# Kernel tuning notes

Measured on AMD Instinct MI355X. Metric: run time of the kernel, lower is better.

The kernel has to match this reference:

```python
import jax, jax.numpy as jnp
import numpy as np

B, C, H, W = 8, 512, 64, 64
HID = 4 * C  # MixFFN hidden = in_dim*4
FOCUS = 3.0


def _ln(x, g, b, eps=1e-5):
    m = x.mean(-1, keepdims=True)
    v = ((x - m) ** 2).mean(-1, keepdims=True)
    return (x - m) / jnp.sqrt(v + eps) * g + b


def setup_inputs() -> dict:
    key = jax.random.key(0)
    ks = jax.random.split(key, 12)
    init = lambda k, shape, fan: (jax.random.normal(k, shape, jnp.float32) / np.float32(np.sqrt(fan)))
    d = {}
    d['x'] = jax.random.normal(ks[0], (B, C, H, W), jnp.float32)
    # 1x1 conv weights stored as (Cout, Cin)
    d['Wq'] = init(ks[1], (C, C), C); d['bq'] = jnp.zeros((C,), jnp.float32)
    d['Wk'] = init(ks[2], (C, C), C); d['bk'] = jnp.zeros((C,), jnp.float32)
    d['Wv'] = init(ks[3], (C, C), C); d['bv'] = jnp.zeros((C,), jnp.float32)
    d['scale'] = jnp.zeros((1, 1, C), jnp.float32)  # nn.Parameter(torch.zeros)
    # MixFFN_skip params
    d['fc1_w'] = init(ks[4], (C, HID), C); d['fc1_b'] = jnp.zeros((HID,), jnp.float32)
    d['dw_w'] = init(ks[5], (HID, 1, 3, 3), 9); d['dw_b'] = jnp.zeros((HID,), jnp.float32)
    d['fc2_w'] = init(ks[6], (HID, C), HID); d['fc2_b'] = jnp.zeros((C,), jnp.float32)
    d['ln1_g'] = jnp.ones((HID,), jnp.float32); d['ln1_b'] = jnp.zeros((HID,), jnp.float32)
    d['lnm_g'] = jnp.ones((C,), jnp.float32); d['lnm_b'] = jnp.zeros((C,), jnp.float32)
    return d


def _forward(x, Wq, bq, Wk, bk, Wv, bv, scale, fc1_w, fc1_b, dw_w, dw_b, fc2_w, fc2_b, ln1_g, ln1_b, lnm_g, lnm_b):
    b, c, h, w = x.shape
    n = h * w
    # 1x1 convs (NCHW), then RAW reshape to (B, N, C) as in torch (no permute!)
    conv1 = lambda t, Wm, bm: jnp.einsum('bchw,oc->bohw', t, Wm) + bm[None, :, None, None]
    q = jax.nn.softmax(conv1(x, Wq, bq).reshape(b, n, c), axis=1)
    k = jax.nn.softmax(conv1(x, Wk, bk).reshape(b, n, c), axis=2)
    v = conv1(x, Wv, bv).reshape(b, n, c)
    q = jax.nn.relu(q) + 1e-6
    k = jax.nn.relu(k) + 1e-6
    sc = jax.nn.softplus(scale)
    q = q / sc
    k = k / sc
    q_norm = jnp.linalg.norm(q, axis=-1, keepdims=True)
    k_norm = jnp.linalg.norm(k, axis=-1, keepdims=True)
    q = q ** FOCUS  # focusing_factor <= 6 branch
    k = k ** FOCUS
    q = q / jnp.linalg.norm(q, axis=-1, keepdims=True) * q_norm
    k = k / jnp.linalg.norm(k, axis=-1, keepdims=True) * k_norm
    # num_heads == 1: (b h) n c == b n c
    z = 1.0 / (jnp.einsum('bic,bc->bi', q, k.sum(axis=1)) + 1e-6)
    kv = jnp.einsum('bjc,bjd->bcd', k, v)  # O(N) linear attention summary
    attn = jnp.einsum('bic,bcd,bi->bid', q, kv, z)
    shortcut = jnp.transpose(x, (0, 2, 3, 1)).reshape(b, n, c)  # proper rearrange b c h w -> b (h w) c
    enhanced = shortcut + attn
    # MixFFN_skip(norm_mlp(enhanced), h, w)
    t = _ln(enhanced, lnm_g, lnm_b)
    a = t @ fc1_w + fc1_b  # (B, N, HID)
    ai = jnp.transpose(a, (0, 2, 1)).reshape(b, HID, h, w)
    dw = jax.lax.conv_general_dilated(ai, dw_w, (1, 1), 'SAME',
                                      dimension_numbers=('NCHW', 'OIHW', 'NCHW'),
                                      feature_group_count=HID)
    dw = dw + dw_b[None, :, None, None]
    dw = jnp.transpose(dw.reshape(b, HID, n), (0, 2, 1))
    ax = jax.nn.gelu(_ln(dw + a, ln1_g, ln1_b), approximate=False)
    mlp_out = ax @ fc2_w + fc2_b
    out = enhanced + mlp_out
    return out.reshape(b, h, w, c)


def reference(x, Wq, bq, Wk, bk, Wv, bv, scale, fc1_w, fc1_b, dw_w, dw_b, fc2_w, fc2_b, ln1_g, ln1_b, lnm_g, lnm_b):
    return _forward(x, Wq, bq, Wk, bk, Wv, bv, scale, fc1_w, fc1_b, dw_w, dw_b, fc2_w, fc2_b, ln1_g, ln1_b, lnm_g, lnm_b)
```

## Files before the change

### kernel.cpp

```cpp
#include <hip/hip_runtime.h>
#include <hip/hip_bf16.h>

typedef __hip_bfloat16 bf16;
typedef __attribute__((ext_vector_type(8))) short bh8;
typedef __attribute__((ext_vector_type(4))) float f32x4;

#define CDIM 512
#define NDIM 4096
#define HIDD 2048
#define BATCH 8

__device__ __forceinline__ float bf2f(short s) {
    union { unsigned u; float f; } c; c.u = ((unsigned)(unsigned short)s) << 16; return c.f;
}
__device__ __forceinline__ short f2bf(float f) {
    union { __hip_bfloat16 h; short s; } c; c.h = __float2bfloat16(f); return c.s;
}
__device__ __forceinline__ float wsum(float v) {
#pragma unroll
    for (int o = 32; o; o >>= 1) v += __shfl_xor(v, o);
    return v;
}
__device__ __forceinline__ float wmax(float v) {
#pragma unroll
    for (int o = 32; o; o >>= 1) v = fmaxf(v, __shfl_xor(v, o));
    return v;
}

#define GLL(g, l) __builtin_amdgcn_global_load_lds( \
    (const __attribute__((address_space(1))) unsigned int*)(g), \
    (__attribute__((address_space(3))) unsigned int*)(l), 16, 0, 0)


__device__ __forceinline__ void stage_ht(const bf16* __restrict__ base, int ld,
                                         int kt, char* ldsb, int t) {
#pragma unroll
    for (int l = 0; l < 2; ++l) {
        const int id = l * 512 + t;
        const int row = id >> 3, c = id & 7;
        const int cs = c ^ (row & 7);
        GLL(base + (long)row * ld + kt + (cs << 3),
            ldsb + l * 8192 + (t >> 6) * 1024 + (t & 63) * 16);
    }
}

template<int MODE, int MFAST>
__global__ __launch_bounds__(512, 2)
void gemm256(const bf16* __restrict__ A, int lda, long sA,
             const bf16* __restrict__ Bt, int ldb, long sB,
             void* __restrict__ Cp, int ldc, long sC, int K,
             const float* __restrict__ bias,
             void* __restrict__ aux1, void* __restrict__ aux2)
{
    __shared__ __align__(16) bf16 smem[65536];
    char* smemB = (char*)smem;
    int bx, by, bz;
    {
        const int gx = gridDim.x, gy = gridDim.y;
        const int nwg = gx * gy * gridDim.z;
        int lid = blockIdx.x + gx * (blockIdx.y + gy * blockIdx.z);
        const int cpx = nwg >> 3;
        int swz = (lid & 7) * cpx + (lid >> 3);
        if constexpr (MFAST) {
            by = swz % gy; swz /= gy;
            bx = swz % gx;
            bz = swz / gx;
        } else {
            bx = swz % gx; swz /= gx;
            by = swz % gy;
            bz = swz / gy;
        }
    }
    const bf16* Ab = A + (long)bz * sA + (long)by * 256 * lda;
    const bf16* Bb = Bt + (long)bz * sB + (long)bx * 256 * ldb;
    const int t = threadIdx.x, lane = t & 63, wid = t >> 6;
    const int wm = wid >> 2, wn = wid & 3;
    const int lg = lane >> 4, lr = lane & 15;

    f32x4 acc[8][4];
#pragma unroll
    for (int m = 0; m < 8; ++m)
#pragma unroll
        for (int n = 0; n < 4; ++n) acc[m][n] = (f32x4){0.f, 0.f, 0.f, 0.f};

    const int T = K >> 6;
    stage_ht(Bb, ldb, 0, smemB + 65536, t);
    stage_ht(Bb + (long)128 * ldb, ldb, 0, smemB + 65536 + 16384, t);
    stage_ht(Ab, lda, 0, smemB, t);
    stage_ht(Ab + (long)128 * lda, lda, 0, smemB + 16384, t);

    for (int tt = 0; tt < T; ++tt) {
        const int cur = tt & 1, nb = cur ^ 1;
        const int ktn = (tt + 1) << 6;
        const bool pf = (tt + 1 < T);
        const int aco = cur ? 16384 : 0;
        const int bco = 32768 + (cur ? 16384 : 0);
        const int anb = nb ? 32768 : 0;
        const int bnb = 65536 + (nb ? 32768 : 0);

        bh8 afA[4], afB[4], bfA[4], bfB[4];

        if (pf) stage_ht(Bb, ldb, ktn, smemB + bnb, t);
        if (pf) asm volatile("s_waitcnt vmcnt(2)" ::: "memory");
        else    asm volatile("s_waitcnt vmcnt(0)" ::: "memory");
        __builtin_amdgcn_s_barrier();
#pragma unroll
        for (int m = 0; m < 4; ++m) {
            const int row = wm * 128 + m * 16 + lr;
            afA[m] = *(const bh8*)(smem + aco + row * 64 + (lg ^ (row & 7)) * 8);
        }
#pragma unroll
        for (int n = 0; n < 4; ++n) {
            const int row = wn * 64 + n * 16 + lr;
            bfA[n] = *(const bh8*)(smem + bco + row * 64 + (lg ^ (row & 7)) * 8);
        }
        asm volatile("s_waitcnt lgkmcnt(0)" ::: "memory");
        __builtin_amdgcn_sched_barrier(0);
        __builtin_amdgcn_s_setprio(1);
#pragma unroll
        for (int m = 0; m < 4; ++m)
#pragma unroll
            for (int n = 0; n < 4; ++n)
                acc[m][n] = __builtin_amdgcn_mfma_f32_16x16x32_bf16(afA[m], bfA[n], acc[m][n], 0, 0, 0);
        __builtin_amdgcn_s_setprio(0);
        __builtin_amdgcn_s_barrier();

#pragma unroll
        for (int m = 0; m < 4; ++m) {
            const int row = wm * 128 + 64 + m * 16 + lr;
            afB[m] = *(const bh8*)(smem + aco + row * 64 + (lg ^ (row & 7)) * 8);
        }
        if (pf) stage_ht(Bb + (long)128 * ldb, ldb, ktn, smemB + bnb + 16384, t);
        asm volatile("s_waitcnt lgkmcnt(0)" ::: "memory");
        __builtin_amdgcn_sched_barrier(0);
        __builtin_amdgcn_s_setprio(1);
#pragma unroll
        for (int m = 0; m < 4; ++m)
#pragma unroll
            for (int n = 0; n < 4; ++n)
                acc[4 + m][n] = __builtin_amdgcn_mfma_f32_16x16x32_bf16(afB[m], bfA[n], acc[4 + m][n], 0, 0, 0);
        __builtin_amdgcn_s_setprio(0);
        __builtin_amdgcn_s_barrier();

#pragma unroll
        for (int m = 0; m < 4; ++m) {
            const int row = wm * 128 + m * 16 + lr;
            afA[m] = *(const bh8*)(smem + aco + row * 64 + ((4 + lg) ^ (row & 7)) * 8);
        }
#pragma unroll
        for (int n = 0; n < 4; ++n) {
            const int row = wn * 64 + n * 16 + lr;
            bfB[n] = *(const bh8*)(smem + bco + row * 64 + ((4 + lg) ^ (row & 7)) * 8);
        }
        if (pf) stage_ht(Ab, lda, ktn, smemB + anb, t);
        asm volatile("s_waitcnt lgkmcnt(0)" ::: "memory");
        __builtin_amdgcn_sched_barrier(0);
        __builtin_amdgcn_s_setprio(1);
#pragma unroll
        for (int m = 0; m < 4; ++m)
#pragma unroll
            for (int n = 0; n < 4; ++n)
                acc[m][n] = __builtin_amdgcn_mfma_f32_16x16x32_bf16(afA[m], bfB[n], acc[m][n], 0, 0, 0);
        __builtin_amdgcn_s_setprio(0);
        __builtin_amdgcn_s_barrier();

#pragma unroll
        for (int m = 0; m < 4; ++m) {
            const int row = wm * 128 + 64 + m * 16 + lr;
            afB[m] = *(const bh8*)(smem + aco + row * 64 + ((4 + lg) ^ (row & 7)) * 8);
        }
        if (pf) stage_ht(Ab + (long)128 * lda, lda, ktn, smemB + anb + 16384, t);
        asm volatile("s_waitcnt lgkmcnt(0)" ::: "memory");
        __builtin_amdgcn_sched_barrier(0);
        __builtin_amdgcn_s_setprio(1);
#pragma unroll
        for (int m = 0; m < 4; ++m)
#pragma unroll
            for (int n = 0; n < 4; ++n)
                acc[4 + m][n] = __builtin_amdgcn_mfma_f32_16x16x32_bf16(afB[m], bfB[n], acc[4 + m][n], 0, 0, 0);
        __builtin_amdgcn_s_setprio(0);
        __builtin_amdgcn_s_barrier();
    }

    const int gr0 = by * 256 + wm * 128;
    const int gc0 = bx * 256 + wn * 64;
    if constexpr (MODE == 0) {
        const int which = by >> 1;
        bf16* dst = (which == 0) ? (bf16*)Cp : (which == 1) ? (bf16*)aux1 : (bf16*)aux2;
        dst += (long)bz * sC;
#pragma unroll
        for (int m = 0; m < 8; ++m)
#pragma unroll
            for (int n = 0; n < 4; ++n) {
                const int col = gc0 + n * 16 + lr;
#pragma unroll
                for (int r = 0; r < 4; ++r) {
                    const int grow = gr0 + m * 16 + lg * 4 + r;
                    float v = acc[m][n][r] + bias[grow];
                    if (which == 0) v = __expf(v);
                    dst[(long)(grow - which * 512) * ldc + col] = __float2bfloat16(v);
                }
            }
    } else {
        bf16* dst = (bf16*)Cp + (long)bz * sC;
#pragma unroll
        for (int m = 0; m < 8; ++m)
#pragma unroll
            for (int n = 0; n < 4; ++n) {
                const int col = gc0 + n * 16 + lr;
                const float bc = bias[col];
#pragma unroll
                for (int r = 0; r < 4; ++r) {
                    const int grow = gr0 + m * 16 + lg * 4 + r;
                    dst[(long)grow * ldc + col] = __float2bfloat16(acc[m][n][r] + bc);
                }
            }
    }
}

enum { EP_BF16_BROW = 1, EP_ATTN = 3, EP_BF16_BCOL = 4, EP_OUT = 5 };

template<int MODE, int TM, int MFAST>
__global__ __launch_bounds__(256)
void gemm_bt(const bf16* __restrict__ A, int lda, long sA,
             const bf16* __restrict__ Bt, int ldb, long sB,
             void* __restrict__ Cp, int ldc, long sC, int K,
             const float* __restrict__ bias,
             const void* __restrict__ aux1, long sAux1,
             const void* __restrict__ aux2, long sAux2)
{
    constexpr int MF = TM / 32;
    __shared__ __align__(16) bf16 smem[TM * 64 + 128 * 64];
    bf16* As = smem;
    bf16* Bs = smem + TM * 64;
    int bx, by, bz;
    {
        const int gx = gridDim.x, gy = gridDim.y;
        const int nwg = gx * gy * gridDim.z;
        int lid = blockIdx.x + gx * (blockIdx.y + gy * blockIdx.z);
        const int cpx = nwg >> 3;
        int swz = (lid & 7) * cpx + (lid >> 3);
        if constexpr (MFAST) {
            by = swz % gy; swz /= gy;
            bx = swz % gx;
            bz = swz / gx;
        } else {
            bx = swz % gx; swz /= gx;
            by = swz % gy;
            bz = swz / gy;
        }
    }
    const bf16* Ab = A + (long)bz * sA + (long)by * TM * lda;
    const bf16* Bb = Bt + (long)bz * sB + (long)bx * 128 * ldb;
    const int t = threadIdx.x, lane = t & 63, wid = t >> 6;
    const int wm = wid >> 1, wn = wid & 1, lg = lane >> 4, lr = lane & 15;

    f32x4 acc[MF][4];
#pragma unroll
    for (int m = 0; m < MF; ++m)
#pragma unroll
        for (int n = 0; n < 4; ++n) acc[m][n] = (f32x4){0.f, 0.f, 0.f, 0.f};

    for (int kt = 0; kt < K; kt += 64) {
#pragma unroll
        for (int i = 0; i < MF; ++i) {
            const int ch = i * 256 + t;
            const int row = ch >> 3;
            const int cs = (ch & 7) ^ (row & 7);
            GLL(Ab + (long)row * lda + kt + (cs << 3), (char*)As + i * 4096 + wid * 1024);
        }
#pragma unroll
        for (int i = 0; i < 4; ++i) {
            const int ch = i * 256 + t;
            const int row = ch >> 3;
            const int cs = (ch & 7) ^ (row & 7);
            GLL(Bb + (long)row * ldb + kt + (cs << 3), (char*)Bs + i * 4096 + wid * 1024);
        }
        __syncthreads();
#pragma unroll
        for (int kk = 0; kk < 2; ++kk) {
            bh8 af[MF], bfv[4];
#pragma unroll
            for (int m = 0; m < MF; ++m) {
                const int row = wm * (TM / 2) + m * 16 + lr;
                const int kc = (kk * 4 + lg) ^ (row & 7);
                af[m] = *(const bh8*)(As + row * 64 + kc * 8);
            }
#pragma unroll
            for (int n = 0; n < 4; ++n) {
                const int row = wn * 64 + n * 16 + lr;
                const int kc = (kk * 4 + lg) ^ (row & 7);
                bfv[n] = *(const bh8*)(Bs + row * 64 + kc * 8);
            }
#pragma unroll
            for (int m = 0; m < MF; ++m)
#pragma unroll
                for (int n = 0; n < 4; ++n)
                    acc[m][n] = __builtin_amdgcn_mfma_f32_16x16x32_bf16(af[m], bfv[n], acc[m][n], 0, 0, 0);
        }
        __syncthreads();
    }

    const int gr0 = by * TM + wm * (TM / 2);
    const int gc0 = bx * 128 + wn * 64;
#pragma unroll
    for (int m = 0; m < MF; ++m) {
#pragma unroll
        for (int n = 0; n < 4; ++n) {
            const int gc = gc0 + n * 16 + lr;
#pragma unroll
            for (int r = 0; r < 4; ++r) {
                const int gr = gr0 + m * 16 + lg * 4 + r;
                float v = acc[m][n][r];
                if constexpr (MODE == EP_BF16_BROW) {
                    ((bf16*)Cp + (long)bz * sC)[(long)gr * ldc + gc] = __float2bfloat16(v + bias[gr]);
                } else if constexpr (MODE == EP_ATTN) {
                    const bf16* xg = (const bf16*)aux1 + (long)bz * sAux1;
                    const float* zg = (const float*)aux2 + (long)bz * sAux2;
                    ((float*)Cp + (long)bz * sC)[(long)gr * ldc + gc] =
                        zg[gr] * v + bf2f(*(const short*)(xg + (long)gr * 512 + gc));
                } else if constexpr (MODE == EP_BF16_BCOL) {
                    ((bf16*)Cp + (long)bz * sC)[(long)gr * ldc + gc] = __float2bfloat16(v + bias[gc]);
                } else {
                    float* op = (float*)Cp;
                    const long idx = (long)gr * ldc + gc;
                    op[idx] = v + bias[gc] + ((const float*)aux1)[idx];
                }
            }
        }
    }
}

__global__ __launch_bounds__(256)
void gemm_tn_splitk(const bf16* __restrict__ A, int lda, long sA,
                    const bf16* __restrict__ B, int ldb, long sB,
                    bf16* __restrict__ part)
{
    __shared__ __align__(16) short smem[2 * 64 * 128];
    short* As = smem;
    short* Bs = smem + 64 * 128;
    int bx, by, bzl;
    {
        const int gx = gridDim.x, gy = gridDim.y;
        const int nwg = gx * gy * gridDim.z;
        int lid = blockIdx.x + gx * (blockIdx.y + gy * blockIdx.z);
        const int cpx = nwg >> 3;
        int swz = (lid & 7) * cpx + (lid >> 3);
        bx = swz % gx; swz /= gx;
        by = swz % gy;
        bzl = swz / gy;
    }
    const int bz = bzl >> 2, ks = bzl & 3;
    const bf16* Ab = A + (long)bz * sA + (long)ks * 1024 * lda + by * 128;
    const bf16* Bb = B + (long)bz * sB + (long)ks * 1024 * ldb + bx * 128;
    const int t = threadIdx.x, lane = t & 63, wid = t >> 6;
    const int wm = wid >> 1, wn = wid & 1, lg = lane >> 4, lr = lane & 15;

    f32x4 acc[4][4];
#pragma unroll
    for (int m = 0; m < 4; ++m)
#pragma unroll
        for (int n = 0; n < 4; ++n) acc[m][n] = (f32x4){0.f, 0.f, 0.f, 0.f};

    for (int kt = 0; kt < 1024; kt += 64) {
#pragma unroll
        for (int i = 0; i < 4; ++i) {
            const int ch = i * 256 + t;
            const int row = ch >> 4;
            const int cs = (ch & 15) ^ (((row >> 3) & 3) << 1);
            GLL(Ab + (long)(kt + row) * lda + (cs << 3), (char*)As + i * 4096 + wid * 1024);
            GLL(Bb + (long)(kt + row) * ldb + (cs << 3), (char*)Bs + i * 4096 + wid * 1024);
        }
        __syncthreads();
#pragma unroll
        for (int kk = 0; kk < 2; ++kk) {
            bh8 af[4], bfv[4];
#pragma unroll
            for (int m = 0; m < 4; ++m) {
                const int col = wm * 64 + m * 16 + lr;
#pragma unroll
                for (int u = 0; u < 8; ++u) {
                    const int row = kk * 32 + lg * 8 + u;
                    af[m][u] = As[row * 128 + (((col >> 3) ^ (((row >> 3) & 3) << 1)) << 3) + (col & 7)];
                }
            }
#pragma unroll
            for (int n = 0; n < 4; ++n) {
                const int col = wn * 64 + n * 16 + lr;
#pragma unroll
                for (int u = 0; u < 8; ++u) {
                    const int row = kk * 32 + lg * 8 + u;
                    bfv[n][u] = Bs[row * 128 + (((col >> 3) ^ (((row >> 3) & 3) << 1)) << 3) + (col & 7)];
                }
            }
#pragma unroll
            for (int m = 0; m < 4; ++m)
#pragma unroll
                for (int n = 0; n < 4; ++n)
                    acc[m][n] = __builtin_amdgcn_mfma_f32_16x16x32_bf16(af[m], bfv[n], acc[m][n], 0, 0, 0);
        }
        __syncthreads();
    }

    bf16* Cs = (bf16*)smem;
    bf16* dstb = part + ((long)bzl << 18) + (long)by * 128 * 512;
#pragma unroll
    for (int m = 0; m < 4; ++m)
#pragma unroll
        for (int n = 0; n < 4; ++n)
#pragma unroll
            for (int r = 0; r < 4; ++r) {
                const int row = wm * 64 + m * 16 + lg * 4 + r;
                const int col = wn * 64 + n * 16 + lr;
                Cs[row * 128 + (col ^ (((row >> 2) & 3) << 4))] = __float2bfloat16(acc[m][n][r]);
            }
    __syncthreads();
#pragma unroll
    for (int it = 0; it < 8; ++it) {
        const int id = it * 256 + t;
        const int row = id >> 4, colc = (id & 15) << 3;
        bh8 v = *(const bh8*)(Cs + row * 128 + (colc ^ (((row >> 2) & 3) << 4)));
        *(bh8*)(dstb + (long)row * 512 + bx * 128 + colc) = v;
    }
}

__global__ __launch_bounds__(256)
void k_transpose3(const float* __restrict__ fc1w, bf16* __restrict__ fc1wT,
                  const float* __restrict__ fc2w, bf16* __restrict__ fc2wT,
                  const float* __restrict__ x, bf16* __restrict__ xbT)
{
    __shared__ float tile[64][65];
    const int bid = blockIdx.x;
    const float* s; bf16* d; int Rd, Cd, bx, by;
    if (bid < 256) {
        s = fc1w; d = fc1wT; Rd = 2048; Cd = 512; bx = bid & 31; by = bid >> 5;
    } else if (bid < 512) {
        const int i = bid - 256;
        s = fc2w; d = fc2wT; Rd = 512; Cd = 2048; bx = i & 7; by = i >> 3;
    } else {
        const int i = bid - 512;
        const int bz = i >> 9, j = i & 511;
        bx = j & 63; by = j >> 6;
        const long NC = (long)NDIM * CDIM;
        s = x + (long)bz * NC; d = xbT + (long)bz * NC; Rd = 4096; Cd = 512;
    }
    const int r0 = bx * 64, c0 = by * 64;
    const int t = threadIdx.x;
#pragma unroll 4
    for (int i = 0; i < 16; ++i) {
        int idx = i * 256 + t;
        int a = idx >> 6, b = idx & 63;
        tile[a][b] = s[(long)(c0 + a) * Rd + r0 + b];
    }
    __syncthreads();
#pragma unroll 4
    for (int i = 0; i < 16; ++i) {
        int idx = i * 256 + t;
        int a = idx >> 6, b = idx & 63;
        d[(long)(r0 + a) * Cd + c0 + b] = __float2bfloat16(tile[b][a]);
    }
}

__global__ void k_setup(const float* __restrict__ Wq, const float* __restrict__ Wk,
                        const float* __restrict__ Wv, bf16* __restrict__ oq,
                        bf16* __restrict__ ok, bf16* __restrict__ ov,
                        const float* __restrict__ scale, float* __restrict__ invsc,
                        const float* __restrict__ w, float* __restrict__ wT,
                        const float* __restrict__ bq, const float* __restrict__ bk,
                        const float* __restrict__ bv, float* __restrict__ bqkv) {
    int i = blockIdx.x * 256 + threadIdx.x;
    if (i < 262144) {
        oq[i] = __float2bfloat16(Wq[i]);
        ok[i] = __float2bfloat16(Wk[i]);
        ov[i] = __float2bfloat16(Wv[i]);
    }
    if (i < 512) invsc[i] = 1.0f / log1pf(expf(scale[i]));
    if (i < 1536) bqkv[i] = (i < 512 ? bq[i] : (i < 1024 ? bk[i - 512] : bv[i - 1024]));
    if (i < HIDD * 9) {
        int chn = i / 9, kk = i % 9;
        wT[kk * HIDD + chn] = w[i];
    }
}

__global__ void k_fill(float* o, int n, float v) {
    int i = blockIdx.x * 256 + threadIdx.x; if (i < n) o[i] = v;
}

__global__ __launch_bounds__(256)
void k_colsums(const bf16* __restrict__ qe, const bf16* __restrict__ kb,
               float* __restrict__ qpart, float* __restrict__ kpart) {
    const int xb = blockIdx.x;
    const int ic = blockIdx.y, b = blockIdx.z;
    const int j = (xb & 1) * 256 + threadIdx.x;
    const bf16* src = (xb < 2) ? qe : kb;
    const bf16* p = src + (long)b * (NDIM * CDIM) + (long)ic * 256 * CDIM + j;
    float s = 0.f;
    for (int i = 0; i < 256; ++i) s += bf2f(*(const short*)(p + (long)i * CDIM));
    ((xb < 2) ? qpart : kpart)[((long)b * 16 + ic) * CDIM + j] = s;
}

__global__ __launch_bounds__(256)
void k_red2(const float* __restrict__ qpart, float* __restrict__ qsum,
            const float* __restrict__ kpart, float* __restrict__ ksum) {
    const int idx = blockIdx.x * 256 + threadIdx.x;
    const int which = idx >> 12, r = idx & 4095;
    const int b = r >> 9, c = r & 511;
    const float* src = which ? kpart : qpart;
    float s = 0.f;
#pragma unroll
    for (int jc = 0; jc < 16; ++jc) s += src[((long)(b * 16 + jc)) * CDIM + c];
    (which ? ksum : qsum)[r] = s;
}

__global__ __launch_bounds__(256)
void k_kvqrow(const bf16* __restrict__ part, bf16* __restrict__ kvt,
              const bf16* __restrict__ qe, const float* __restrict__ qsum,
              const float* __restrict__ invsc, bf16* __restrict__ qb,
              const float* __restrict__ ksum, float* __restrict__ z)
{
    if (blockIdx.x < 1024) {
        const long e = ((long)blockIdx.x * 256 + threadIdx.x) * 8;
        const int b = (int)(e >> 18);
        const int off = (int)(e & 262143);
        float s[8] = {0.f, 0.f, 0.f, 0.f, 0.f, 0.f, 0.f, 0.f};
#pragma unroll
        for (int ks = 0; ks < 4; ++ks) {
            bh8 v = *(const bh8*)(part + (((long)(b * 4 + ks)) << 18) + off);
#pragma unroll
            for (int j = 0; j < 8; ++j) s[j] += bf2f(v[j]);
        }
        bh8 o;
#pragma unroll
        for (int j = 0; j < 8; ++j) o[j] = f2bf(s[j]);
        *(bh8*)(kvt + ((long)b << 18) + off) = o;
        return;
    }
    const long row = (long)(blockIdx.x - 1024) * 4 + (threadIdx.x >> 6);
    const int lane = threadIdx.x & 63;
    const int b = (int)(row >> 12);
    bh8 ev = *(const bh8*)(qe + row * CDIM + lane * 8);
    const float* qs = qsum + b * CDIM + lane * 8;
    const float* is = invsc + lane * 8;
    f32x4 s0 = *(const f32x4*)qs, s1 = *(const f32x4*)(qs + 4);
    f32x4 i0 = *(const f32x4*)is, i1 = *(const f32x4*)(is + 4);
    float q[8];
#pragma unroll
    for (int k = 0; k < 4; ++k) {
        q[k]     = (bf2f(ev[k]) / s0[k] + 1e-6f) * i0[k];
        q[k + 4] = (bf2f(ev[k + 4]) / s1[k] + 1e-6f) * i1[k];
    }
    float s2 = 0.f, s6 = 0.f, q3[8];
#pragma unroll
    for (int k = 0; k < 8; ++k) { s2 += q[k] * q[k]; float c = q[k] * q[k] * q[k]; q3[k] = c; s6 += c * c; }
    s2 = wsum(s2); s6 = wsum(s6);
    const float sc = sqrtf(s2) / sqrtf(s6);
    bh8 o;
#pragma unroll
    for (int k = 0; k < 8; ++k) o[k] = f2bf(q3[k] * sc);
    *(bh8*)(qb + row * CDIM + lane * 8) = o;
    const float* ks = ksum + (long)b * CDIM + lane * 8;
    f32x4 k0 = *(const f32x4*)ks, k1 = *(const f32x4*)(ks + 4);
    float zd = 0.f;
#pragma unroll
    for (int j = 0; j < 4; ++j) { zd += bf2f(o[j]) * k0[j]; zd += bf2f(o[j + 4]) * k1[j]; }
    zd = wsum(zd);
    if (lane == 0) z[row] = 1.0f / (zd + 1e-6f);
}

__global__ __launch_bounds__(256)
void k_krow(bf16* __restrict__ kb, const float* __restrict__ invsc)
{
    const long row = (long)blockIdx.x * 4 + (threadIdx.x >> 6);
    const int lane = threadIdx.x & 63;
    bh8 v = *(const bh8*)(kb + row * CDIM + lane * 8);
    const float* is = invsc + lane * 8;
    f32x4 i0 = *(const f32x4*)is, i1 = *(const f32x4*)(is + 4);
    float xv[8];
#pragma unroll
    for (int k = 0; k < 8; ++k) xv[k] = bf2f(v[k]);
    float mx = -1e30f;
#pragma unroll
    for (int k = 0; k < 8; ++k) mx = fmaxf(mx, xv[k]);
    mx = wmax(mx);
    float e[8], se = 0.f;
#pragma unroll
    for (int k = 0; k < 8; ++k) { e[k] = __expf(xv[k] - mx); se += e[k]; }
    se = wsum(se);
    const float inv = 1.0f / se;
    float q[8];
#pragma unroll
    for (int k = 0; k < 4; ++k) {
        q[k]     = (e[k] * inv + 1e-6f) * i0[k];
        q[k + 4] = (e[k + 4] * inv + 1e-6f) * i1[k];
    }
    float s2 = 0.f, s6 = 0.f, q3[8];
#pragma unroll
    for (int k = 0; k < 8; ++k) { s2 += q[k] * q[k]; float c = q[k] * q[k] * q[k]; q3[k] = c; s6 += c * c; }
    s2 = wsum(s2); s6 = wsum(s6);
    const float sc = sqrtf(s2) / sqrtf(s6);
    bh8 o;
#pragma unroll
    for (int k = 0; k < 8; ++k) o[k] = f2bf(q3[k] * sc);
    *(bh8*)(kb + row * CDIM + lane * 8) = o;
}

__global__ __launch_bounds__(256)
void k_ln512(const float* __restrict__ src, const float* __restrict__ g,
             const float* __restrict__ bta, bf16* __restrict__ dst)
{
    const long row = (long)blockIdx.x * 4 + (threadIdx.x >> 6);
    const int lane = threadIdx.x & 63;
    const float* p = src + row * CDIM + lane * 8;
    f32x4 a0 = *(const f32x4*)p, a1 = *(const f32x4*)(p + 4);
    float s = 0.f, ss = 0.f;
#pragma unroll
    for (int k = 0; k < 4; ++k) { s += a0[k] + a1[k]; ss += a0[k] * a0[k] + a1[k] * a1[k]; }
    s = wsum(s); ss = wsum(ss);
    const float mean = s * (1.0f / 512), var = ss * (1.0f / 512) - mean * mean;
    const float rstd = rsqrtf(var + 1e-5f);
    const float* gp = g + lane * 8;
    const float* bp = bta + lane * 8;
    f32x4 g0 = *(const f32x4*)gp, g1 = *(const f32x4*)(gp + 4);
    f32x4 b0 = *(const f32x4*)bp, b1 = *(const f32x4*)(bp + 4);
    bh8 o;
#pragma unroll
    for (int k = 0; k < 4; ++k) {
        o[k]     = f2bf((a0[k] - mean) * rstd * g0[k] + b0[k]);
        o[k + 4] = f2bf((a1[k] - mean) * rstd * g1[k] + b1[k]);
    }
    *(bh8*)(dst + row * CDIM + lane * 8) = o;
}

__global__ __launch_bounds__(256)
void k_dwlngelu4(const bf16* __restrict__ a, const float* __restrict__ dwwT,
                 const float* __restrict__ dwb, const float* __restrict__ g1,
                 const float* __restrict__ b1, bf16* __restrict__ ax)
{
    const long s0 = (long)blockIdx.x * 4;
    const int h = (int)((s0 >> 6) & 63);
    const int w0 = (int)(s0 & 63);
    const int ch = threadIdx.x * 8;

    float wgt[9][8];
#pragma unroll
    for (int kk = 0; kk < 9; ++kk) {
        f32x4 w0v = *(const f32x4*)(dwwT + kk * HIDD + ch);
        f32x4 w1v = *(const f32x4*)(dwwT + kk * HIDD + ch + 4);
#pragma unroll
        for (int j = 0; j < 4; ++j) { wgt[kk][j] = w0v[j]; wgt[kk][j + 4] = w1v[j]; }
    }
#pragma unroll
    for (int j = 0; j < 8; ++j) wgt[4][j] += 1.0f;

    float acc[4][8];
    {
        f32x4 d0 = *(const f32x4*)(dwb + ch), d1 = *(const f32x4*)(dwb + ch + 4);
#pragma unroll
        for (int ti = 0; ti < 4; ++ti)
#pragma unroll
            for (int j = 0; j < 4; ++j) { acc[ti][j] = d0[j]; acc[ti][j + 4] = d1[j]; }
    }

#pragma unroll
    for (int dy = -1; dy <= 1; ++dy) {
        const int hh = h + dy;
        if ((unsigned)hh >= 64u) continue;
#pragma unroll
        for (int c = -1; c <= 4; ++c) {
            const int ww = w0 + c;
            if ((unsigned)ww >= 64u) continue;
            bh8 v = *(const bh8*)(a + (s0 + (long)dy * 64 + c) * HIDD + ch);
            float f[8];
#pragma unroll
            for (int j = 0; j < 8; ++j) f[j] = bf2f(v[j]);
#pragma unroll
            for (int ti = 0; ti < 4; ++ti) {
                const int dx = c - ti;
                if (dx < -1 || dx > 1) continue;
                const int kk = (dy + 1) * 3 + (dx + 1);
#pragma unroll
                for (int j = 0; j < 8; ++j) acc[ti][j] += wgt[kk][j] * f[j];
            }
        }
    }

    float sv[4], qv[4];
#pragma unroll
    for (int ti = 0; ti < 4; ++ti) {
        float s = 0.f, q = 0.f;
#pragma unroll
        for (int j = 0; j < 8; ++j) { s += acc[ti][j]; q += acc[ti][j] * acc[ti][j]; }
        sv[ti] = wsum(s); qv[ti] = wsum(q);
    }
    __shared__ float red[4][4][2];
    const int wid = threadIdx.x >> 6, lane = threadIdx.x & 63;
    if (lane == 0)
#pragma unroll
        for (int ti = 0; ti < 4; ++ti) { red[wid][ti][0] = sv[ti]; red[wid][ti][1] = qv[ti]; }
    __syncthreads();

    f32x4 ga = *(const f32x4*)(g1 + ch), gb = *(const f32x4*)(g1 + ch + 4);
    f32x4 ba = *(const f32x4*)(b1 + ch), bb = *(const f32x4*)(b1 + ch + 4);
    float gg[8], bb8[8];
#pragma unroll
    for (int j = 0; j < 4; ++j) { gg[j] = ga[j]; gg[j + 4] = gb[j]; bb8[j] = ba[j]; bb8[j + 4] = bb[j]; }

#pragma unroll
    for (int ti = 0; ti < 4; ++ti) {
        const float s = red[0][ti][0] + red[1][ti][0] + red[2][ti][0] + red[3][ti][0];
        const float q = red[0][ti][1] + red[1][ti][1] + red[2][ti][1] + red[3][ti][1];
        const float mean = s * (1.0f / 2048), var = q * (1.0f / 2048) - mean * mean;
        const float rstd = rsqrtf(var + 1e-5f);
        bh8 o;
#pragma unroll
        for (int j = 0; j < 8; ++j) {
            float y = (acc[ti][j] - mean) * rstd * gg[j] + bb8[j];
            o[j] = f2bf(0.5f * y * (1.0f + erff(y * 0.70710678118654752f)));
        }
        *(bh8*)(ax + (s0 + ti) * HIDD + ch) = o;
    }
}

extern "C" void kernel_launch(void* const* d_in, const int* in_sizes, int n_in,
                              void* d_out, int out_size, void* d_ws, size_t ws_size,
                              hipStream_t stream) {
    const float* x     = (const float*)d_in[0];
    const float* Wq    = (const float*)d_in[1];
    const float* bq    = (const float*)d_in[2];
    const float* Wk    = (const float*)d_in[3];
    const float* bk    = (const float*)d_in[4];
    const float* Wv    = (const float*)d_in[5];
    const float* bv    = (const float*)d_in[6];
    const float* scale = (const float*)d_in[7];
    const float* fc1_w = (const float*)d_in[8];
    const float* fc1_b = (const float*)d_in[9];
    const float* dw_w  = (const float*)d_in[10];
    const float* dw_b  = (const float*)d_in[11];
    const float* fc2_w = (const float*)d_in[12];
    const float* fc2_b = (const float*)d_in[13];
    const float* ln1_g = (const float*)d_in[14];
    const float* ln1_b = (const float*)d_in[15];
    const float* lnm_g = (const float*)d_in[16];
    const float* lnm_b = (const float*)d_in[17];
    float* out = (float*)d_out;
    char* p = (char*)d_ws;

    bf16*  xbT   = (bf16*)(p + 0);
    bf16*  kb    = (bf16*)(p + 33554432);
    bf16*  vb    = (bf16*)(p + 67108864);
    bf16*  kvt   = (bf16*)(p + 100663296);
    bf16*  wqb   = (bf16*)(p + 104857600);
    bf16*  wkb   = (bf16*)(p + 105381888);
    bf16*  wvb   = (bf16*)(p + 105906176);
    bf16*  fc1wT = (bf16*)(p + 106430464);
    bf16*  fc2wT = (bf16*)(p + 108527616);
    float* invsc = (float*)(p + 110624768);
    float* dwwT  = (float*)(p + 110626816);
    float* bqkv  = (float*)(p + 110700544);
    float* qsum  = (float*)(p + 110757888);
    float* ksum  = (float*)(p + 110905344);
    float* zbuf  = (float*)(p + 110921728);
    const size_t REQUIRED = 111052800;
    float* qpart = (float*)kvt;
    float* kpart = (float*)((char*)kvt + 262144);
    bf16*  qe    = (bf16*)out;
    bf16*  kvpart= (bf16*)((char*)out + 33554432);
    bf16*  qb    = kb;
    bf16*  abuf  = (bf16*)(p + 0);
    bf16*  axbuf = (bf16*)(p + 33554432);
    bf16*  tbuf  = (bf16*)(p + 67108864);

    if (ws_size < REQUIRED) {
        k_fill<<<(out_size + 255) / 256, 256, 0, stream>>>(out, out_size, 100000.0f + (float)(ws_size >> 20));
        return;
    }

    const long NC = (long)NDIM * CDIM;

    k_setup<<<1024, 256, 0, stream>>>(Wq, Wk, Wv, wqb, wkb, wvb, scale, invsc,
                                      dw_w, dwwT, bq, bk, bv, bqkv);
    k_transpose3<<<4608, 256, 0, stream>>>(fc1_w, fc1wT, fc2_w, fc2wT, x, xbT);

    gemm256<0, 1><<<dim3(16, 6, 8), 512, 0, stream>>>(
        wqb, 512, 0, xbT, 512, NC, qe, 4096, NC, 512, bqkv, kb, vb);

    k_krow<<<8192, 256, 0, stream>>>(kb, invsc);
    k_colsums<<<dim3(4, 16, 8), 256, 0, stream>>>(qe, kb, qpart, kpart);
    k_red2<<<32, 256, 0, stream>>>(qpart, qsum, kpart, ksum);

    gemm_tn_splitk<<<dim3(4, 4, 32), 256, 0, stream>>>(vb, 512, NC, kb, 512, NC, kvpart);
    k_kvqrow<<<9216, 256, 0, stream>>>(kvpart, kvt, qe, qsum, invsc, qb, ksum, zbuf);

    gemm_bt<EP_ATTN, 128, 0><<<dim3(4, 32, 8), 256, 0, stream>>>(
        qb, 512, NC, kvt, 512, 262144, out, 512, NC, 512, nullptr, xbT, NC, zbuf, 4096);

    k_ln512<<<8192, 256, 0, stream>>>(out, lnm_g, lnm_b, tbuf);
    for (int q4 = 0; q4 < 4; ++q4) {
        float* outq = out + (long)q4 * 8192 * CDIM;
        bf16* tq = tbuf + (long)q4 * 8192 * CDIM;
        gemm256<1, 0><<<dim3(8, 32, 1), 512, 0, stream>>>(
            tq, 512, 0, fc1wT, 512, 0, abuf, 2048, 0, 512, fc1_b, nullptr, nullptr);
        k_dwlngelu4<<<2048, 256, 0, stream>>>(abuf, dwwT, dw_b, ln1_g, ln1_b, axbuf);
        gemm_bt<EP_OUT, 64, 0><<<dim3(4, 128, 1), 256, 0, stream>>>(
            axbuf, 2048, 0, fc2wT, 2048, 0, outq, 512, 0, 2048, fc2_b, outq, 0, nullptr, 0);
    }
}
```

Baseline: 573.9 us.

## Stage GEMM epilogue through LDS, fuse K column sums, use gemm256 for attention

The gemm256 bf16 epilogue now writes results into swizzled shared memory and then stores them as 16-byte vector rows, replacing scattered 2-byte global stores. The K softmax/focus kernel now processes 8 rows per wave and also produces per-block column partial sums, so the separate column-sum pass over K is dropped. k_red2 reduces the larger set of K partials instead. The attention output GEMM moves from gemm_bt to gemm256 with a new mode-2 epilogue that applies z and adds the residual, at the cost of a small grid (256 blocks) and uncoalesced scalar epilogue stores.

```diff
diff --git a/kernel.cpp b/kernel.cpp
--- a/kernel.cpp
+++ b/kernel.cpp
@@ -184,10 +184,10 @@
 
     const int gr0 = by * 256 + wm * 128;
     const int gc0 = bx * 256 + wn * 64;
-    if constexpr (MODE == 0) {
-        const int which = by >> 1;
-        bf16* dst = (which == 0) ? (bf16*)Cp : (which == 1) ? (bf16*)aux1 : (bf16*)aux2;
-        dst += (long)bz * sC;
+    if constexpr (MODE == 2) {
+        const bf16* xg = (const bf16*)aux1 + (long)bz * ((long)NDIM * CDIM);
+        const float* zg = (const float*)aux2 + (long)bz * NDIM;
+        float* op = (float*)Cp + (long)bz * sC;
 #pragma unroll
         for (int m = 0; m < 8; ++m)
 #pragma unroll
@@ -196,25 +196,45 @@
 #pragma unroll
                 for (int r = 0; r < 4; ++r) {
                     const int grow = gr0 + m * 16 + lg * 4 + r;
-                    float v = acc[m][n][r] + bias[grow];
-                    if (which == 0) v = __expf(v);
-                    dst[(long)(grow - which * 512) * ldc + col] = __float2bfloat16(v);
+                    op[(long)grow * ldc + col] =
+                        zg[grow] * acc[m][n][r] + bf2f(*(const short*)(xg + (long)grow * 512 + col));
                 }
             }
     } else {
-        bf16* dst = (bf16*)Cp + (long)bz * sC;
+        bf16* Cs = smem;
+        const int which = (MODE == 0) ? (by >> 1) : 0;
 #pragma unroll
         for (int m = 0; m < 8; ++m)
 #pragma unroll
-            for (int n = 0; n < 4; ++n) {
-                const int col = gc0 + n * 16 + lr;
-                const float bc = bias[col];
+            for (int n = 0; n < 4; ++n)
 #pragma unroll
                 for (int r = 0; r < 4; ++r) {
-                    const int grow = gr0 + m * 16 + lg * 4 + r;
-                    dst[(long)grow * ldc + col] = __float2bfloat16(acc[m][n][r] + bc);
+                    const int row = wm * 128 + m * 16 + lg * 4 + r;
+                    const int col = wn * 64 + n * 16 + lr;
+                    float v = acc[m][n][r];
+                    if constexpr (MODE == 0) {
+                        v += bias[by * 256 + row];
+                        if (which == 0) v = __expf(v);
+                    } else {
+                        v += bias[bx * 256 + col];
+                    }
+                    Cs[row * 256 + (col ^ (((row >> 2) & 3) << 4))] = __float2bfloat16(v);
                 }
-            }
+        __syncthreads();
+        bf16* dstb;
+        if constexpr (MODE == 0) {
+            dstb = (which == 0) ? (bf16*)Cp : (which == 1) ? (bf16*)aux1 : (bf16*)aux2;
+            dstb += (long)bz * sC + (long)((by & 1) * 256) * ldc;
+        } else {
+            dstb = (bf16*)Cp + (long)bz * sC + (long)by * 256 * ldc;
+        }
+#pragma unroll
+        for (int it = 0; it < 16; ++it) {
+            const int id = it * 512 + t;
+            const int row = id >> 5, colc = (id & 31) << 3;
+            bh8 v = *(const bh8*)(Cs + row * 256 + (colc ^ (((row >> 2) & 3) << 4)));
+            *(bh8*)(dstb + (long)row * ldc + bx * 256 + colc) = v;
+        }
     }
 }
 
@@ -487,16 +507,13 @@
 }
 
 __global__ __launch_bounds__(256)
-void k_colsums(const bf16* __restrict__ qe, const bf16* __restrict__ kb,
-               float* __restrict__ qpart, float* __restrict__ kpart) {
-    const int xb = blockIdx.x;
+void k_colsums(const bf16* __restrict__ qe, float* __restrict__ qpart) {
     const int ic = blockIdx.y, b = blockIdx.z;
-    const int j = (xb & 1) * 256 + threadIdx.x;
-    const bf16* src = (xb < 2) ? qe : kb;
-    const bf16* p = src + (long)b * (NDIM * CDIM) + (long)ic * 256 * CDIM + j;
+    const int j = blockIdx.x * 256 + threadIdx.x;
+    const bf16* p = qe + (long)b * (NDIM * CDIM) + (long)ic * 256 * CDIM + j;
     float s = 0.f;
     for (int i = 0; i < 256; ++i) s += bf2f(*(const short*)(p + (long)i * CDIM));
-    ((xb < 2) ? qpart : kpart)[((long)b * 16 + ic) * CDIM + j] = s;
+    qpart[((long)b * 16 + ic) * CDIM + j] = s;
 }
 
 __global__ __launch_bounds__(256)
@@ -505,11 +522,70 @@
     const int idx = blockIdx.x * 256 + threadIdx.x;
     const int which = idx >> 12, r = idx & 4095;
     const int b = r >> 9, c = r & 511;
-    const float* src = which ? kpart : qpart;
     float s = 0.f;
-#pragma unroll
-    for (int jc = 0; jc < 16; ++jc) s += src[((long)(b * 16 + jc)) * CDIM + c];
-    (which ? ksum : qsum)[r] = s;
+    if (which == 0) {
+#pragma unroll
+        for (int jc = 0; jc < 16; ++jc) s += qpart[((long)(b * 16 + jc)) * CDIM + c];
+        qsum[r] = s;
+    } else {
+        for (int jc = 0; jc < 128; ++jc) s += kpart[((long)(b * 128 + jc)) * CDIM + c];
+        ksum[r] = s;
+    }
+}
+
+__global__ __launch_bounds__(256)
+void k_krow2(bf16* __restrict__ kb, const float* __restrict__ invsc,
+             float* __restrict__ kpart)
+{
+    const int lane = threadIdx.x & 63, wid = threadIdx.x >> 6;
+    const float* is = invsc + lane * 8;
+    f32x4 i0 = *(const f32x4*)is, i1 = *(const f32x4*)(is + 4);
+    float kacc[8] = {0.f, 0.f, 0.f, 0.f, 0.f, 0.f, 0.f, 0.f};
+    const long base = (long)blockIdx.x * 32 + wid * 8;
+    for (int rr = 0; rr < 8; ++rr) {
+        const long row = base + rr;
+        bh8 v = *(const bh8*)(kb + row * CDIM + lane * 8);
+        float xv[8];
+#pragma unroll
+        for (int k = 0; k < 8; ++k) xv[k] = bf2f(v[k]);
+        float mx = -1e30f;
+#pragma unroll
+        for (int k = 0; k < 8; ++k) mx = fmaxf(mx, xv[k]);
+        mx = wmax(mx);
+        float e[8], se = 0.f;
+#pragma unroll
+        for (int k = 0; k < 8; ++k) { e[k] = __expf(xv[k] - mx); se += e[k]; }
+        se = wsum(se);
+        const float inv = 1.0f / se;
+        float q[8];
+#pragma unroll
+        for (int k = 0; k < 4; ++k) {
+            q[k]     = (e[k] * inv + 1e-6f) * i0[k];
+            q[k + 4] = (e[k + 4] * inv + 1e-6f) * i1[k];
+        }
+        float s2 = 0.f, s6 = 0.f, q3[8];
+#pragma unroll
+        for (int k = 0; k < 8; ++k) { s2 += q[k] * q[k]; float c = q[k] * q[k] * q[k]; q3[k] = c; s6 += c * c; }
+        s2 = wsum(s2); s6 = wsum(s6);
+        const float sc = sqrtf(s2) / sqrtf(s6);
+        bh8 o;
+#pragma unroll
+        for (int k = 0; k < 8; ++k) {
+            o[k] = f2bf(q3[k] * sc);
+            kacc[k] += bf2f(o[k]);
+        }
+        *(bh8*)(kb + row * CDIM + lane * 8) = o;
+    }
+    __shared__ float red[4][512];
+#pragma unroll
+    for (int k = 0; k < 8; ++k) red[wid][lane * 8 + k] = kacc[k];
+    __syncthreads();
+    const int c0 = threadIdx.x * 2;
+#pragma unroll
+    for (int u = 0; u < 2; ++u) {
+        const int c = c0 + u;
+        kpart[(long)blockIdx.x * 512 + c] = red[0][c] + red[1][c] + red[2][c] + red[3][c];
+    }
 }
 
 __global__ __launch_bounds__(256)
@@ -565,43 +641,6 @@
     for (int j = 0; j < 4; ++j) { zd += bf2f(o[j]) * k0[j]; zd += bf2f(o[j + 4]) * k1[j]; }
     zd = wsum(zd);
     if (lane == 0) z[row] = 1.0f / (zd + 1e-6f);
-}
-
-__global__ __launch_bounds__(256)
-void k_krow(bf16* __restrict__ kb, const float* __restrict__ invsc)
-{
-    const long row = (long)blockIdx.x * 4 + (threadIdx.x >> 6);
-    const int lane = threadIdx.x & 63;
-    bh8 v = *(const bh8*)(kb + row * CDIM + lane * 8);
-    const float* is = invsc + lane * 8;
-    f32x4 i0 = *(const f32x4*)is, i1 = *(const f32x4*)(is + 4);
-    float xv[8];
-#pragma unroll
-    for (int k = 0; k < 8; ++k) xv[k] = bf2f(v[k]);
-    float mx = -1e30f;
-#pragma unroll
-    for (int k = 0; k < 8; ++k) mx = fmaxf(mx, xv[k]);
-    mx = wmax(mx);
-    float e[8], se = 0.f;
-#pragma unroll
-    for (int k = 0; k < 8; ++k) { e[k] = __expf(xv[k] - mx); se += e[k]; }
-    se = wsum(se);
-    const float inv = 1.0f / se;
-    float q[8];
-#pragma unroll
-    for (int k = 0; k < 4; ++k) {
-        q[k]     = (e[k] * inv + 1e-6f) * i0[k];
-        q[k + 4] = (e[k + 4] * inv + 1e-6f) * i1[k];
-    }
-    float s2 = 0.f, s6 = 0.f, q3[8];
-#pragma unroll
-    for (int k = 0; k < 8; ++k) { s2 += q[k] * q[k]; float c = q[k] * q[k] * q[k]; q3[k] = c; s6 += c * c; }
-    s2 = wsum(s2); s6 = wsum(s6);
-    const float sc = sqrtf(s2) / sqrtf(s6);
-    bh8 o;
-#pragma unroll
-    for (int k = 0; k < 8; ++k) o[k] = f2bf(q3[k] * sc);
-    *(bh8*)(kb + row * CDIM + lane * 8) = o;
 }
 
 __global__ __launch_bounds__(256)
@@ -784,15 +823,15 @@
     gemm256<0, 1><<<dim3(16, 6, 8), 512, 0, stream>>>(
         wqb, 512, 0, xbT, 512, NC, qe, 4096, NC, 512, bqkv, kb, vb);
 
-    k_krow<<<8192, 256, 0, stream>>>(kb, invsc);
-    k_colsums<<<dim3(4, 16, 8), 256, 0, stream>>>(qe, kb, qpart, kpart);
+    k_krow2<<<1024, 256, 0, stream>>>(kb, invsc, kpart);
+    k_colsums<<<dim3(2, 16, 8), 256, 0, stream>>>(qe, qpart);
     k_red2<<<32, 256, 0, stream>>>(qpart, qsum, kpart, ksum);
 
     gemm_tn_splitk<<<dim3(4, 4, 32), 256, 0, stream>>>(vb, 512, NC, kb, 512, NC, kvpart);
     k_kvqrow<<<9216, 256, 0, stream>>>(kvpart, kvt, qe, qsum, invsc, qb, ksum, zbuf);
 
-    gemm_bt<EP_ATTN, 128, 0><<<dim3(4, 32, 8), 256, 0, stream>>>(
-        qb, 512, NC, kvt, 512, 262144, out, 512, NC, 512, nullptr, xbT, NC, zbuf, 4096);
+    gemm256<2, 0><<<dim3(2, 16, 8), 512, 0, stream>>>(
+        qb, 512, NC, kvt, 512, 262144, out, 512, NC, 512, nullptr, xbT, zbuf);
 
     k_ln512<<<8192, 256, 0, stream>>>(out, lnm_g, lnm_b, tbuf);
     for (int q4 = 0; q4 < 4; ++q4) {
```

Measured after the change: 587.2 us. 1.02x slower.
